# Optimization experiments

Measured on AMD Instinct MI355X. Metric: run time of the kernel, lower is better.

Reference implementation:

```python
import jax, jax.numpy as jnp
import numpy as np

B, C, H, W = 32, 384, 28, 28
E, HID, K = 4, 384, 2  # HID = hidden_features(1536) // num_experts(4)


def setup_inputs() -> dict:
    key = jax.random.key(0)
    ks = jax.random.split(key, 5)
    x = jax.random.normal(ks[0], (B, C, H, W), jnp.float32)
    gate_w = jax.random.normal(ks[1], (C, E), jnp.float32) * 0.02
    gate_b = jnp.zeros((E,), jnp.float32)
    w1 = jax.random.normal(ks[2], (E, HID, C), jnp.float32) * 0.02
    b1 = jnp.zeros((E, HID), jnp.float32)
    w2 = jax.random.normal(ks[3], (E, C, HID), jnp.float32) * 0.02
    b2 = jnp.zeros((E, C), jnp.float32)
    return {"x": x, "gate_w": gate_w, "gate_b": gate_b,
            "w1": w1, "b1": b1, "w2": w2, "b2": b2}


def reference(x, gate_w, gate_b, w1, b1, w2, b2):
    b, c, h, w = x.shape
    e = gate_b.shape[0]
    # per-token gating: tokens are spatial positions in NHWC order
    x_flat = x.transpose(0, 2, 3, 1).reshape(-1, c)          # [N, C], N = B*H*W
    scores = jax.nn.softmax(x_flat @ gate_w + gate_b, -1)    # [N, E]
    top_v, top_i = jax.lax.top_k(scores, K)                  # [N, K]
    top_w = jax.nn.softmax(top_v, -1)                        # [N, K] renormalized
    # weight map per top-k slot: [K, B, H, W]
    wmap = top_w.T.reshape(K, b, h, w)
    # faithful to torch loop: expert i contributes at slot k iff ANY token routed
    # to it at slot k; the weight applied is the UNMASKED slot-k weight map.
    present = (top_i[:, :, None] == jnp.arange(e)[None, None, :]).any(0)  # [K, E]
    coef = jnp.einsum('ke,kbhw->ebhw', present.astype(x.dtype), wmap)     # [E, B, H, W]
    # dense per-expert 1x1-conv MLP over the FULL tensor (as in the source)
    hdn = jax.nn.relu(jnp.einsum('bchw,edc->ebdhw', x, w1)
                      + b1[:, None, :, None, None])          # [E, B, HID, H, W]
    y = jnp.einsum('ebdhw,eod->ebohw', hdn, w2) + b2[:, None, :, None, None]
    out = jnp.einsum('ebohw,ebhw->bohw', y, coef)            # [B, C, H, W]
    return out
```

## Files before the change

### kernel.cpp

```cpp
#include <hip/hip_runtime.h>
#include <hip/hip_bf16.h>
#include <stdint.h>

#define B_DIM 32
#define C_DIM 384
#define HW_DIM 784
#define E_DIM 4
#define HID_DIM 384
#define NTOK (B_DIM * HW_DIM)
#define NH (E_DIM * HID_DIM)
#define WSZ 589824

using short8 = __attribute__((ext_vector_type(8))) short;
using f32x4  = __attribute__((ext_vector_type(4))) float;
typedef unsigned short ushort_t;

__device__ __forceinline__ ushort_t f2bf(float f) {
  __hip_bfloat16 h = __float2bfloat16(f);
  return __builtin_bit_cast(ushort_t, h);
}

__device__ __forceinline__ void gload_lds16(const void* g, void* l) {
  __builtin_amdgcn_global_load_lds(
      (const __attribute__((address_space(1))) unsigned int*)g,
      (__attribute__((address_space(3))) unsigned int*)l, 16, 0, 0);
}

__global__ __launch_bounds__(256) void prep_kernel(
    const float* __restrict__ w1, const float* __restrict__ w2,
    ushort_t* __restrict__ W1b, ushort_t* __restrict__ W2f,
    unsigned int* __restrict__ present) {
  int i = blockIdx.x * 256 + threadIdx.x;
  if (i == 0) *present = 0u;
  if (i >= WSZ) return;
  W1b[i] = f2bf(w1[i]);
  {
    int r = i;
    const int nt = r / 196608; r -= nt * 196608;
    const int ks = r / 4096;   r -= ks * 4096;
    const int wn = r >> 11;
    const int ni = (r >> 9) & 3;
    const int ln = (r >> 3) & 63;
    const int tt = r & 7;
    const int o = nt * 128 + wn * 64 + ni * 16 + (ln & 15);
    const int kg = ks * 32 + (ln >> 4) * 8 + tt;
    const int e = kg / HID_DIM, d = kg - e * HID_DIM;
    W2f[i] = f2bf(w2[((size_t)e * C_DIM + o) * HID_DIM + d]);
  }
}

__global__ __launch_bounds__(512) void gate_kernel(
    const float* __restrict__ x, const float* __restrict__ gw,
    const float* __restrict__ gb, ushort_t* __restrict__ xb,
    float* __restrict__ topw, unsigned int* __restrict__ present) {
  __shared__ __align__(16) ushort_t lxs[64][392];
  __shared__ float pscore[8][64][4];
  __shared__ unsigned int pmask;
  const int b = blockIdx.x;
  const int p0 = blockIdx.y * 64;
  const int cnt = min(64, HW_DIM - p0);
  const int tid = threadIdx.x;
  const int cg = tid >> 6, tl = tid & 63;
  if (tid == 0) pmask = 0u;
  float a0 = 0.f, a1 = 0.f, a2 = 0.f, a3 = 0.f;
  const bool valid = tl < cnt;
  if (valid) {
    const float* xp = x + (size_t)b * C_DIM * HW_DIM + p0 + tl;
    for (int c = cg; c < C_DIM; c += 8) {
      const float v = xp[(size_t)c * HW_DIM];
      lxs[tl][c] = f2bf(v);
      const float4 g = *(const float4*)&gw[c * 4];
      a0 += v * g.x; a1 += v * g.y; a2 += v * g.z; a3 += v * g.w;
    }
  }
  pscore[cg][tl][0] = a0; pscore[cg][tl][1] = a1;
  pscore[cg][tl][2] = a2; pscore[cg][tl][3] = a3;
  __syncthreads();
  if (cg == 0 && valid) {
    float z[4];
#pragma unroll
    for (int e = 0; e < 4; e++) {
      float s = gb[e];
#pragma unroll
      for (int g8 = 0; g8 < 8; g8++) s += pscore[g8][tl][e];
      z[e] = s;
    }
    const float mx = fmaxf(fmaxf(z[0], z[1]), fmaxf(z[2], z[3]));
    float s[4]; float sum = 0.f;
#pragma unroll
    for (int e = 0; e < 4; e++) { s[e] = __expf(z[e] - mx); sum += s[e]; }
    const float inv = 1.f / sum;
#pragma unroll
    for (int e = 0; e < 4; e++) s[e] *= inv;
    int e0 = 0; float v0 = s[0];
#pragma unroll
    for (int e = 1; e < 4; e++) if (s[e] > v0) { v0 = s[e]; e0 = e; }
    int e1 = -1; float v1 = -1.f;
#pragma unroll
    for (int e = 0; e < 4; e++) if (e != e0 && s[e] > v1) { v1 = s[e]; e1 = e; }
    const float r = __expf(v1 - v0);
    const float w0 = 1.f / (1.f + r);
    const int m = b * HW_DIM + p0 + tl;
    topw[m * 2] = w0;
    topw[m * 2 + 1] = 1.f - w0;
    atomicOr(&pmask, (1u << e0) | (1u << (4 + e1)));
  }
  __syncthreads();
  if (tid == 0) atomicOr(present, pmask);
  const int nchunk = cnt * 48;
  for (int ci = tid; ci < nchunk; ci += 512) {
    const int row = ci / 48, c8 = ci - row * 48;
    short8 v = *(const short8*)&lxs[row][c8 * 8];
    *(short8*)&xb[(size_t)(b * HW_DIM + p0 + row) * C_DIM + c8 * 8] = v;
  }
}

__global__ __launch_bounds__(256, 3) void gemm_1b(
    const ushort_t* __restrict__ A, const ushort_t* __restrict__ Bw,
    const float* __restrict__ bias, const float* __restrict__ topw,
    const unsigned int* __restrict__ presentp, ushort_t* __restrict__ hOut) {
  constexpr int KDIM = C_DIM, BM = 128, BN = 128, BK = 32;
  constexpr int KT = KDIM / BK;
  constexpr int NTN = NH / BN;
  constexpr int ASZ = BM * BK;
  __shared__ ushort_t smem[6 * ASZ];

  const int nwg = NTN * (NTOK / BM);
  const int orig = blockIdx.x;
  const int xcd = orig & 7;
  const int qq = nwg >> 3, rr = nwg & 7;
  const int wg = (xcd < rr ? xcd * (qq + 1) : rr * (qq + 1) + (xcd - rr) * qq)
               + (orig >> 3);
  const int mt = wg / NTN, nt = wg % NTN;
  const int m0 = mt * BM, n0 = nt * BN;

  const int tid = threadIdx.x;
  const int lane = tid & 63;
  const int wid = tid >> 6;
  const int wm = wid >> 1, wn = wid & 1;
  const int lanel = lane & 15, laneq = lane >> 4;

  auto stage = [&](int t) {
    const int buf = t % 3;
    ushort_t* dstA = smem + buf * ASZ;
    ushort_t* dstB = smem + 3 * ASZ + buf * ASZ;
    const int kb = t * BK;
#pragma unroll
    for (int li = 0; li < 2; ++li) {
      const int P = (li * 256 + tid) * 16;
      const int row = P >> 6;
      const int cb = (P & 63) ^ (((row >> 1) & 3) << 4);
      gload_lds16(&A[(size_t)(m0 + row) * KDIM + kb + (cb >> 1)],
                  (char*)dstA + P);
    }
#pragma unroll
    for (int li = 0; li < 2; ++li) {
      const int P = (li * 256 + tid) * 16;
      const int row = P >> 6;
      const int cb = (P & 63) ^ (((row >> 1) & 3) << 4);
      gload_lds16(&Bw[(size_t)(n0 + row) * KDIM + kb + (cb >> 1)],
                  (char*)dstB + P);
    }
  };

  f32x4 acc[4][4] = {};
  const int cbr = (laneq * 16) ^ (((lanel >> 1) & 3) << 4);

  stage(0);
  stage(1);
  for (int t = 0; t < KT; ++t) {
    if (t + 1 < KT)
      asm volatile("s_waitcnt vmcnt(4)" ::: "memory");
    else
      asm volatile("s_waitcnt vmcnt(0)" ::: "memory");
    __builtin_amdgcn_sched_barrier(0);
    __builtin_amdgcn_s_barrier();
    __builtin_amdgcn_sched_barrier(0);
    if (t + 2 < KT) stage(t + 2);
    const int buf = t % 3;
    const char* Ab = (const char*)(smem + buf * ASZ) + (wm * 64 + lanel) * 64;
    const char* Bb =
        (const char*)(smem + 3 * ASZ + buf * ASZ) + (wn * 64 + lanel) * 64;
    short8 av[4], bv[4];
#pragma unroll
    for (int i = 0; i < 4; ++i) av[i] = *(const short8*)(Ab + i * 1024 + cbr);
#pragma unroll
    for (int j = 0; j < 4; ++j) bv[j] = *(const short8*)(Bb + j * 1024 + cbr);
    __builtin_amdgcn_s_setprio(1);
#pragma unroll
    for (int i = 0; i < 4; ++i)
#pragma unroll
      for (int j = 0; j < 4; ++j)
        acc[i][j] = __builtin_amdgcn_mfma_f32_16x16x32_bf16(
            av[i], bv[j], acc[i][j], 0, 0, 0);
    __builtin_amdgcn_s_setprio(0);
  }

  const unsigned int pm = *presentp;
  __syncthreads();
  ushort_t* tr = smem;
  const int e = n0 / HID_DIM;
  const float P0 = (float)((pm >> e) & 1u);
  const float P1 = (float)((pm >> (4 + e)) & 1u);
#pragma unroll
  for (int mi = 0; mi < 4; ++mi) {
    const int r0 = wm * 64 + mi * 16 + laneq * 4;
    const int mg = m0 + r0;
    const float4 t0 = *(const float4*)&topw[mg * 2];
    const float4 t1 = *(const float4*)&topw[mg * 2 + 4];
    const float cj[4] = {P0 * t0.x + P1 * t0.y, P0 * t0.z + P1 * t0.w,
                         P0 * t1.x + P1 * t1.y, P0 * t1.z + P1 * t1.w};
#pragma unroll
    for (int ni = 0; ni < 4; ++ni) {
      const int cl = wn * 64 + ni * 16 + lanel;
      const float bvv = bias[n0 + cl];
#pragma unroll
      for (int j = 0; j < 4; ++j) {
        float v = fmaxf(acc[mi][ni][j] + bvv, 0.f);
        tr[(r0 + j) * 128 + cl] = f2bf(cj[j] * v);
      }
    }
  }
  __syncthreads();
#pragma unroll
  for (int it = 0; it < 8; ++it) {
    const int c = it * 256 + tid;
    const int row = c >> 4, cr = c & 15;
    *(short8*)&hOut[(size_t)(m0 + row) * NH + n0 + cr * 8] =
        *(const short8*)&tr[row * 128 + cr * 8];
  }
}

__global__ __launch_bounds__(128, 2) void gemm_bd(
    const ushort_t* __restrict__ A, const ushort_t* __restrict__ Wf,
    const float* __restrict__ bias, const float* __restrict__ topw,
    const unsigned int* __restrict__ presentp, float* __restrict__ outp) {
  constexpr int KDIM = NH, BM = 128, BN = 128, BK = 32;
  constexpr int KT = KDIM / BK;
  constexpr int NTN = C_DIM / BN;
  constexpr int ASZ = BM * BK;
  __shared__ ushort_t smem[3 * ASZ];

  const int nwg = NTN * (NTOK / BM);
  const int orig = blockIdx.x;
  const int xcd = orig & 7;
  const int qq = nwg >> 3, rr = nwg & 7;
  const int wg = (xcd < rr ? xcd * (qq + 1) : rr * (qq + 1) + (xcd - rr) * qq)
               + (orig >> 3);
  const int mt = wg / NTN, nt = wg % NTN;
  const int m0 = mt * BM, n0 = nt * BN;

  const int tid = threadIdx.x;
  const int lane = tid & 63;
  const int wn = tid >> 6;
  const int lanel = lane & 15, laneq = lane >> 4;

  const ushort_t* wbase = Wf + (size_t)nt * KT * 4096 + wn * 2048 + lane * 8;

  auto stage = [&](int t) {
    ushort_t* dst = smem + (t % 3) * ASZ;
    const int kb = t * BK;
#pragma unroll
    for (int li = 0; li < 4; ++li) {
      const int P = (li * 128 + tid) * 16;
      const int row = P >> 6;
      const int cb = (P & 63) ^ (((row >> 1) & 3) << 4);
      gload_lds16(&A[(size_t)(m0 + row) * KDIM + kb + (cb >> 1)],
                  (char*)dst + P);
    }
  };
  auto ldB = [&](int t, short8* bv) {
    const ushort_t* p = wbase + (size_t)t * 4096;
#pragma unroll
    for (int j = 0; j < 4; ++j) bv[j] = *(const short8*)(p + j * 512);
  };

  f32x4 acc[8][4] = {};
  const int cbr = (laneq * 16) ^ (((lanel >> 1) & 3) << 4);

  short8 bvA[4], bvB[4];

  auto step = [&](int t, short8* cur) {
    if (t + 1 < KT)
      asm volatile("s_waitcnt vmcnt(10)" ::: "memory");
    else
      asm volatile("s_waitcnt vmcnt(4)" ::: "memory");
    __builtin_amdgcn_sched_barrier(0);
    __builtin_amdgcn_s_barrier();
    __builtin_amdgcn_sched_barrier(0);
    if (t + 2 < KT) stage(t + 2);
    const char* Ab = (const char*)(smem + (t % 3) * ASZ) + lanel * 64;
    short8 av[8];
#pragma unroll
    for (int i = 0; i < 8; ++i) av[i] = *(const short8*)(Ab + i * 1024 + cbr);
    __builtin_amdgcn_s_setprio(1);
#pragma unroll
    for (int i = 0; i < 8; ++i)
#pragma unroll
      for (int j = 0; j < 4; ++j)
        acc[i][j] = __builtin_amdgcn_mfma_f32_16x16x32_bf16(
            av[i], cur[j], acc[i][j], 0, 0, 0);
    __builtin_amdgcn_s_setprio(0);
    if (t + 2 < KT) ldB(t + 2, cur);
  };

  stage(0);
  ldB(0, bvA);
  stage(1);
  ldB(1, bvB);
  for (int t = 0; t < KT; t += 2) {
    step(t, bvA);
    step(t + 1, bvB);
  }

  const unsigned int pm = *presentp;
  float B0[4], B1[4];
#pragma unroll
  for (int ni = 0; ni < 4; ++ni) {
    const int o = n0 + wn * 64 + ni * 16 + lanel;
    float s0 = 0.f, s1 = 0.f;
#pragma unroll
    for (int e2 = 0; e2 < 4; ++e2) {
      const float bb = bias[e2 * C_DIM + o];
      s0 += (float)((pm >> e2) & 1u) * bb;
      s1 += (float)((pm >> (4 + e2)) & 1u) * bb;
    }
    B0[ni] = s0; B1[ni] = s1;
  }
#pragma unroll
  for (int mi = 0; mi < 8; ++mi) {
    const int mg = m0 + mi * 16 + laneq * 4;
    const float4 t0 = *(const float4*)&topw[mg * 2];
    const float4 t1 = *(const float4*)&topw[mg * 2 + 4];
    const int bb2 = mg / HW_DIM;
    const int p = mg - bb2 * HW_DIM;
#pragma unroll
    for (int ni = 0; ni < 4; ++ni) {
      const int o = n0 + wn * 64 + ni * 16 + lanel;
      float4 v;
      v.x = acc[mi][ni][0] + t0.x * B0[ni] + t0.y * B1[ni];
      v.y = acc[mi][ni][1] + t0.z * B0[ni] + t0.w * B1[ni];
      v.z = acc[mi][ni][2] + t1.x * B0[ni] + t1.y * B1[ni];
      v.w = acc[mi][ni][3] + t1.z * B0[ni] + t1.w * B1[ni];
      *(float4*)&outp[((size_t)bb2 * C_DIM + o) * HW_DIM + p] = v;
    }
  }
}

extern "C" void kernel_launch(void* const* d_in, const int* in_sizes, int n_in,
                              void* d_out, int out_size, void* d_ws, size_t ws_size,
                              hipStream_t stream) {
  const float* x  = (const float*)d_in[0];
  const float* gw = (const float*)d_in[1];
  const float* gb = (const float*)d_in[2];
  const float* w1 = (const float*)d_in[3];
  const float* b1 = (const float*)d_in[4];
  const float* w2 = (const float*)d_in[5];
  const float* b2 = (const float*)d_in[6];
  float* out = (float*)d_out;

  char* ws = (char*)d_ws;
  ushort_t* xb = (ushort_t*)ws;   ws += (size_t)NTOK * C_DIM * 2;
  ushort_t* hdnS = (ushort_t*)ws; ws += (size_t)NTOK * NH * 2;
  ushort_t* W1b = (ushort_t*)ws;  ws += (size_t)WSZ * 2;
  ushort_t* W2f = (ushort_t*)ws;  ws += (size_t)WSZ * 2;
  float* topw = (float*)ws;       ws += (size_t)NTOK * 2 * 4;
  unsigned int* present = (unsigned int*)ws;

  prep_kernel<<<dim3(WSZ / 256), dim3(256), 0, stream>>>(
      w1, w2, W1b, W2f, present);
  gate_kernel<<<dim3(B_DIM, 13), dim3(512), 0, stream>>>(
      x, gw, gb, xb, topw, present);
  gemm_1b<<<dim3((NTOK / 128) * (NH / 128)), dim3(256), 0, stream>>>(
      xb, W1b, b1, topw, present, hdnS);
  gemm_bd<<<dim3((NTOK / 128) * (C_DIM / 128)), dim3(128), 0, stream>>>(
      hdnS, W2f, b2, topw, present, out);
}
```

Before: 116.7 us.

## Split-K the second GEMM into two halves with a separate reduction kernel

```diff
diff --git a/kernel.cpp b/kernel.cpp
--- a/kernel.cpp
+++ b/kernel.cpp
@@ -231,22 +231,28 @@
   }
 }
 
-__global__ __launch_bounds__(128, 2) void gemm_bd(
+__global__ __launch_bounds__(128, 3) void gemm_bd(
     const ushort_t* __restrict__ A, const ushort_t* __restrict__ Wf,
     const float* __restrict__ bias, const float* __restrict__ topw,
-    const unsigned int* __restrict__ presentp, float* __restrict__ outp) {
+    const unsigned int* __restrict__ presentp, float* __restrict__ outp,
+    float* __restrict__ pout1, int split) {
   constexpr int KDIM = NH, BM = 128, BN = 128, BK = 32;
-  constexpr int KT = KDIM / BK;
+  constexpr int KTFULL = KDIM / BK;
   constexpr int NTN = C_DIM / BN;
   constexpr int ASZ = BM * BK;
   __shared__ ushort_t smem[3 * ASZ];
 
+  const int orig = blockIdx.x;
+  const int sub = split ? (orig >> 1) : orig;
+  const int half = split ? (orig & 1) : 0;
+  const int nsteps = split ? (KTFULL / 2) : KTFULL;
+  const int ks0 = half * nsteps;
+
   const int nwg = NTN * (NTOK / BM);
-  const int orig = blockIdx.x;
-  const int xcd = orig & 7;
+  const int xcd = sub & 7;
   const int qq = nwg >> 3, rr = nwg & 7;
   const int wg = (xcd < rr ? xcd * (qq + 1) : rr * (qq + 1) + (xcd - rr) * qq)
-               + (orig >> 3);
+               + (sub >> 3);
   const int mt = wg / NTN, nt = wg % NTN;
   const int m0 = mt * BM, n0 = nt * BN;
 
@@ -255,11 +261,12 @@
   const int wn = tid >> 6;
   const int lanel = lane & 15, laneq = lane >> 4;
 
-  const ushort_t* wbase = Wf + (size_t)nt * KT * 4096 + wn * 2048 + lane * 8;
+  const ushort_t* wbase =
+      Wf + (size_t)nt * KTFULL * 4096 + wn * 2048 + lane * 8;
 
   auto stage = [&](int t) {
     ushort_t* dst = smem + (t % 3) * ASZ;
-    const int kb = t * BK;
+    const int kb = (ks0 + t) * BK;
 #pragma unroll
     for (int li = 0; li < 4; ++li) {
       const int P = (li * 128 + tid) * 16;
@@ -270,7 +277,7 @@
     }
   };
   auto ldB = [&](int t, short8* bv) {
-    const ushort_t* p = wbase + (size_t)t * 4096;
+    const ushort_t* p = wbase + (size_t)(ks0 + t) * 4096;
 #pragma unroll
     for (int j = 0; j < 4; ++j) bv[j] = *(const short8*)(p + j * 512);
   };
@@ -281,14 +288,14 @@
   short8 bvA[4], bvB[4];
 
   auto step = [&](int t, short8* cur) {
-    if (t + 1 < KT)
+    if (t + 1 < nsteps)
       asm volatile("s_waitcnt vmcnt(10)" ::: "memory");
     else
       asm volatile("s_waitcnt vmcnt(4)" ::: "memory");
     __builtin_amdgcn_sched_barrier(0);
     __builtin_amdgcn_s_barrier();
     __builtin_amdgcn_sched_barrier(0);
-    if (t + 2 < KT) stage(t + 2);
+    if (t + 2 < nsteps) stage(t + 2);
     const char* Ab = (const char*)(smem + (t % 3) * ASZ) + lanel * 64;
     short8 av[8];
 #pragma unroll
@@ -301,49 +308,80 @@
         acc[i][j] = __builtin_amdgcn_mfma_f32_16x16x32_bf16(
             av[i], cur[j], acc[i][j], 0, 0, 0);
     __builtin_amdgcn_s_setprio(0);
-    if (t + 2 < KT) ldB(t + 2, cur);
+    if (t + 2 < nsteps) ldB(t + 2, cur);
   };
 
   stage(0);
   ldB(0, bvA);
   stage(1);
   ldB(1, bvB);
-  for (int t = 0; t < KT; t += 2) {
+  for (int t = 0; t < nsteps; t += 2) {
     step(t, bvA);
     step(t + 1, bvB);
   }
 
-  const unsigned int pm = *presentp;
-  float B0[4], B1[4];
-#pragma unroll
-  for (int ni = 0; ni < 4; ++ni) {
-    const int o = n0 + wn * 64 + ni * 16 + lanel;
-    float s0 = 0.f, s1 = 0.f;
-#pragma unroll
-    for (int e2 = 0; e2 < 4; ++e2) {
-      const float bb = bias[e2 * C_DIM + o];
-      s0 += (float)((pm >> e2) & 1u) * bb;
-      s1 += (float)((pm >> (4 + e2)) & 1u) * bb;
-    }
-    B0[ni] = s0; B1[ni] = s1;
-  }
-#pragma unroll
-  for (int mi = 0; mi < 8; ++mi) {
-    const int mg = m0 + mi * 16 + laneq * 4;
-    const float4 t0 = *(const float4*)&topw[mg * 2];
-    const float4 t1 = *(const float4*)&topw[mg * 2 + 4];
-    const int bb2 = mg / HW_DIM;
-    const int p = mg - bb2 * HW_DIM;
+  if (half == 0) {
+    const unsigned int pm = *presentp;
+    float B0[4], B1[4];
 #pragma unroll
     for (int ni = 0; ni < 4; ++ni) {
       const int o = n0 + wn * 64 + ni * 16 + lanel;
-      float4 v;
-      v.x = acc[mi][ni][0] + t0.x * B0[ni] + t0.y * B1[ni];
-      v.y = acc[mi][ni][1] + t0.z * B0[ni] + t0.w * B1[ni];
-      v.z = acc[mi][ni][2] + t1.x * B0[ni] + t1.y * B1[ni];
-      v.w = acc[mi][ni][3] + t1.z * B0[ni] + t1.w * B1[ni];
-      *(float4*)&outp[((size_t)bb2 * C_DIM + o) * HW_DIM + p] = v;
-    }
+      float s0 = 0.f, s1 = 0.f;
+#pragma unroll
+      for (int e2 = 0; e2 < 4; ++e2) {
+        const float bb = bias[e2 * C_DIM + o];
+        s0 += (float)((pm >> e2) & 1u) * bb;
+        s1 += (float)((pm >> (4 + e2)) & 1u) * bb;
+      }
+      B0[ni] = s0; B1[ni] = s1;
+    }
+#pragma unroll
+    for (int mi = 0; mi < 8; ++mi) {
+      const int mg = m0 + mi * 16 + laneq * 4;
+      const float4 t0 = *(const float4*)&topw[mg * 2];
+      const float4 t1 = *(const float4*)&topw[mg * 2 + 4];
+      const int bb2 = mg / HW_DIM;
+      const int p = mg - bb2 * HW_DIM;
+#pragma unroll
+      for (int ni = 0; ni < 4; ++ni) {
+        const int o = n0 + wn * 64 + ni * 16 + lanel;
+        float4 v;
+        v.x = acc[mi][ni][0] + t0.x * B0[ni] + t0.y * B1[ni];
+        v.y = acc[mi][ni][1] + t0.z * B0[ni] + t0.w * B1[ni];
+        v.z = acc[mi][ni][2] + t1.x * B0[ni] + t1.y * B1[ni];
+        v.w = acc[mi][ni][3] + t1.z * B0[ni] + t1.w * B1[ni];
+        *(float4*)&outp[((size_t)bb2 * C_DIM + o) * HW_DIM + p] = v;
+      }
+    }
+  } else {
+#pragma unroll
+    for (int mi = 0; mi < 8; ++mi) {
+      const int mg = m0 + mi * 16 + laneq * 4;
+      const int bb2 = mg / HW_DIM;
+      const int p = mg - bb2 * HW_DIM;
+#pragma unroll
+      for (int ni = 0; ni < 4; ++ni) {
+        const int o = n0 + wn * 64 + ni * 16 + lanel;
+        float4 v;
+        v.x = acc[mi][ni][0];
+        v.y = acc[mi][ni][1];
+        v.z = acc[mi][ni][2];
+        v.w = acc[mi][ni][3];
+        *(float4*)&pout1[((size_t)bb2 * C_DIM + o) * HW_DIM + p] = v;
+      }
+    }
+  }
+}
+
+__global__ __launch_bounds__(256) void reduce_kernel(
+    float* __restrict__ out, const float* __restrict__ p1) {
+  const size_t n4 = (size_t)NTOK * C_DIM / 4;
+  const size_t stride = (size_t)gridDim.x * 256;
+  for (size_t i = blockIdx.x * 256 + threadIdx.x; i < n4; i += stride) {
+    float4 a = ((const float4*)out)[i];
+    const float4 b = ((const float4*)p1)[i];
+    a.x += b.x; a.y += b.y; a.z += b.z; a.w += b.w;
+    ((float4*)out)[i] = a;
   }
 }
 
@@ -365,7 +403,11 @@
   ushort_t* W1b = (ushort_t*)ws;  ws += (size_t)WSZ * 2;
   ushort_t* W2f = (ushort_t*)ws;  ws += (size_t)WSZ * 2;
   float* topw = (float*)ws;       ws += (size_t)NTOK * 2 * 4;
-  unsigned int* present = (unsigned int*)ws;
+  unsigned int* present = (unsigned int*)ws; ws += 256;
+  float* pout1 = (float*)ws;      ws += (size_t)NTOK * C_DIM * 4;
+
+  const size_t needed = (size_t)(ws - (char*)d_ws);
+  const int split = (ws_size >= needed) ? 1 : 0;
 
   prep_kernel<<<dim3(WSZ / 256), dim3(256), 0, stream>>>(
       w1, w2, W1b, W2f, present);
@@ -373,6 +415,9 @@
       x, gw, gb, xb, topw, present);
   gemm_1b<<<dim3((NTOK / 128) * (NH / 128)), dim3(256), 0, stream>>>(
       xb, W1b, b1, topw, present, hdnS);
-  gemm_bd<<<dim3((NTOK / 128) * (C_DIM / 128)), dim3(128), 0, stream>>>(
-      hdnS, W2f, b2, topw, present, out);
-}
+  const int g2 = (NTOK / 128) * (C_DIM / 128);
+  gemm_bd<<<dim3(split ? 2 * g2 : g2), dim3(128), 0, stream>>>(
+      hdnS, W2f, b2, topw, present, out, pout1, split);
+  if (split)
+    reduce_kernel<<<dim3(2048), dim3(256), 0, stream>>>(out, pout1);
+}
```

Result: slower. 326.9 us (+180.3%).
